# Kernel tuning notes

Measured on AMD Instinct MI355X. Metric: run time of the kernel, lower is better.

The kernel has to match this reference:

```python
import jax, jax.numpy as jnp
import numpy as np

B, N_BG, F = 512, 10000, 32
H = 128  # n_neurons


def setup_inputs() -> dict:
    key = jax.random.key(0)
    ks = jax.random.split(key, 8)
    s = lambda fan_in: 1.0 / np.sqrt(fan_in)
    return {
        "X": jax.random.normal(ks[0], (B, F), dtype=jnp.float32),
        "x_background": jax.random.normal(ks[1], (N_BG, F), dtype=jnp.float32),
        "y_background": jax.random.normal(ks[2], (N_BG, 1), dtype=jnp.float32),
        "W0": jax.random.normal(ks[3], (F, H), dtype=jnp.float32) * s(F),
        "b0": jnp.zeros((H,), dtype=jnp.float32),
        "W1": jax.random.normal(ks[4], (H, H), dtype=jnp.float32) * s(H),
        "b1": jnp.zeros((H,), dtype=jnp.float32),
        "Wout": jax.random.normal(ks[5], (H, F), dtype=jnp.float32) * s(H),
        "bout": jnp.zeros((F,), dtype=jnp.float32),
    }


def reference(X, x_background, y_background, W0, b0, W1, b1, Wout, bout):
    # MLPDistModel.get_b_vectors: 2 hidden ReLU layers + linear head, out_size = F
    h = jax.nn.relu(X @ W0 + b0)            # [B, H]
    h = jax.nn.relu(h @ W1 + b1)            # [B, H]
    b_vec = h @ Wout + bout                 # [B, F] (b_vectors squeezed from [B,1,F])
    # Nadaraya-Watson: weighted L1 distance to every background point
    diff = jnp.abs(X[:, None, :] - x_background[None, :, :])   # [B, N_bg, F]
    distances = jnp.sum(jnp.abs(b_vec)[:, None, :] * diff, axis=-1)  # [B, N_bg]
    weights = jnp.exp(-distances)
    weights_norm = weights / jnp.sum(weights, axis=1, keepdims=True)
    # y_background.swapaxes(0,1): [1, N_bg]; weighted average over background set
    out = jnp.sum(y_background.T * weights_norm, axis=1, keepdims=True)  # [B, 1]
    return out
```

## Files before the change

### kernel.cpp

```cpp
#include <hip/hip_runtime.h>

#define B      512
#define NBG    10000
#define F      32
#define H      128
#define PTS    20
#define NPG    500
#define RB     4
#define MLPBLK (B / RB)

__device__ __forceinline__ float qsum(float v) {
    int a = __builtin_amdgcn_update_dpp(0, __float_as_int(v), 0xB1, 0xF, 0xF, true);
    float v1 = v + __int_as_float(a);
    int b = __builtin_amdgcn_update_dpp(0, __float_as_int(v1), 0x4E, 0xF, 0xF, true);
    return v1 + __int_as_float(b);
}
__device__ __forceinline__ float psum1(float v) {
    int a = __builtin_amdgcn_update_dpp(0, __float_as_int(v), 0xB1, 0xF, 0xF, true);
    return v + __int_as_float(a);
}

__global__ __launch_bounds__(128) void prep_kernel(
    const float* __restrict__ X,
    const float* __restrict__ W0, const float* __restrict__ b0,
    const float* __restrict__ W1, const float* __restrict__ b1,
    const float* __restrict__ Wout, const float* __restrict__ bout,
    float* __restrict__ babsR)
{
    __shared__ __align__(16) float xr[RB * F];
    __shared__ __align__(16) float h0[RB * H];
    __shared__ __align__(16) float h1[RB * H];
    const int t  = threadIdx.x;
    const int r0 = blockIdx.x * RB;

    for (int i = t; i < RB * F; i += 128) {
        int r = i >> 5, f = i & 31;
        xr[r * F + f] = X[(r0 + r) * F + f];
    }
    __syncthreads();

    float acc[RB];
    #pragma unroll
    for (int r = 0; r < RB; ++r) acc[r] = b0[t];
    #pragma unroll
    for (int f4 = 0; f4 < F / 4; ++f4) {
        float wa = W0[(4*f4+0)*H + t];
        float wb = W0[(4*f4+1)*H + t];
        float wc = W0[(4*f4+2)*H + t];
        float wd = W0[(4*f4+3)*H + t];
        #pragma unroll
        for (int r = 0; r < RB; ++r) {
            float4 xv = *(const float4*)&xr[r * F + 4*f4];
            acc[r] += xv.x*wa + xv.y*wb + xv.z*wc + xv.w*wd;
        }
    }
    #pragma unroll
    for (int r = 0; r < RB; ++r) h0[r * H + t] = fmaxf(acc[r], 0.f);
    __syncthreads();

    #pragma unroll
    for (int r = 0; r < RB; ++r) acc[r] = b1[t];
    #pragma unroll 8
    for (int j4 = 0; j4 < H / 4; ++j4) {
        float wa = W1[(4*j4+0)*H + t];
        float wb = W1[(4*j4+1)*H + t];
        float wc = W1[(4*j4+2)*H + t];
        float wd = W1[(4*j4+3)*H + t];
        #pragma unroll
        for (int r = 0; r < RB; ++r) {
            float4 hv = *(const float4*)&h0[r * H + 4*j4];
            acc[r] += hv.x*wa + hv.y*wb + hv.z*wc + hv.w*wd;
        }
    }
    #pragma unroll
    for (int r = 0; r < RB; ++r) h1[r * H + t] = fmaxf(acc[r], 0.f);
    __syncthreads();

    for (int i = t; i < RB * F; i += 128) {
        int r = i >> 5, f = i & 31;
        float a = bout[f];
        #pragma unroll 8
        for (int j4 = 0; j4 < H / 4; ++j4) {
            float4 hv = *(const float4*)&h1[r * H + 4*j4];
            a += hv.x*Wout[(4*j4+0)*F + f] + hv.y*Wout[(4*j4+1)*F + f]
               + hv.z*Wout[(4*j4+2)*F + f] + hv.w*Wout[(4*j4+3)*F + f];
        }
        babsR[(r0 + r) * F + f] = fabsf(a);
    }
}

__global__ __launch_bounds__(256) void nw_partial(
    const float* __restrict__ X,
    const float* __restrict__ babsR,
    const float* __restrict__ xbg,
    const float* __restrict__ ybg,
    float* __restrict__ psw,
    float* __restrict__ pswy)
{
    __shared__ __align__(16) float ttp[PTS / 2 * F * 2];
    const int tid = threadIdx.x;
    const int fg  = tid & 3;
    const int bs  = tid >> 2;
    const int b0i = blockIdx.y * 128 + bs;
    const int b1i = b0i + 64;
    const int n0  = blockIdx.x * PTS;

    for (int i = tid; i < PTS * F; i += 256) {
        int nr = i >> 5, f = i & 31;
        ttp[(nr >> 1) * 64 + f * 2 + (nr & 1)] = xbg[n0 * F + i];
    }

    const float4 xqA0 = *(const float4*)&X[b0i * F + fg * 8];
    const float4 xqB0 = *(const float4*)&X[b0i * F + fg * 8 + 4];
    const float4 xqA1 = *(const float4*)&X[b1i * F + fg * 8];
    const float4 xqB1 = *(const float4*)&X[b1i * F + fg * 8 + 4];
    const float4 bvA0 = *(const float4*)&babsR[b0i * F + fg * 8];
    const float4 bvB0 = *(const float4*)&babsR[b0i * F + fg * 8 + 4];
    const float4 bvA1 = *(const float4*)&babsR[b1i * F + fg * 8];
    const float4 bvB1 = *(const float4*)&babsR[b1i * F + fg * 8 + 4];
    __syncthreads();

    const float4* t4 = (const float4*)ttp;
    float swp = 0.f, swyp = 0.f;

    #pragma unroll
    for (int jq = 0; jq < PTS / 4; ++jq) {
        const float4 yv = *(const float4*)&ybg[n0 + jq * 4];
        #pragma unroll
        for (int jj = 0; jj < 2; ++jj) {
            const int jp = jq * 2 + jj;
            const int base = jp * 16 + fg * 4;
            float d00 = 0.f, d10 = 0.f, d01 = 0.f, d11 = 0.f;
            {
                float4 v0 = t4[base + 0];
                float4 v1 = t4[base + 1];
                d00 += bvA0.x * fabsf(xqA0.x - v0.x);
                d10 += bvA0.x * fabsf(xqA0.x - v0.y);
                d01 += bvA1.x * fabsf(xqA1.x - v0.x);
                d11 += bvA1.x * fabsf(xqA1.x - v0.y);
                d00 += bvA0.y * fabsf(xqA0.y - v0.z);
                d10 += bvA0.y * fabsf(xqA0.y - v0.w);
                d01 += bvA1.y * fabsf(xqA1.y - v0.z);
                d11 += bvA1.y * fabsf(xqA1.y - v0.w);
                d00 += bvA0.z * fabsf(xqA0.z - v1.x);
                d10 += bvA0.z * fabsf(xqA0.z - v1.y);
                d01 += bvA1.z * fabsf(xqA1.z - v1.x);
                d11 += bvA1.z * fabsf(xqA1.z - v1.y);
                d00 += bvA0.w * fabsf(xqA0.w - v1.z);
                d10 += bvA0.w * fabsf(xqA0.w - v1.w);
                d01 += bvA1.w * fabsf(xqA1.w - v1.z);
                d11 += bvA1.w * fabsf(xqA1.w - v1.w);
            }
            {
                float4 v2 = t4[base + 2];
                float4 v3 = t4[base + 3];
                d00 += bvB0.x * fabsf(xqB0.x - v2.x);
                d10 += bvB0.x * fabsf(xqB0.x - v2.y);
                d01 += bvB1.x * fabsf(xqB1.x - v2.x);
                d11 += bvB1.x * fabsf(xqB1.x - v2.y);
                d00 += bvB0.y * fabsf(xqB0.y - v2.z);
                d10 += bvB0.y * fabsf(xqB0.y - v2.w);
                d01 += bvB1.y * fabsf(xqB1.y - v2.z);
                d11 += bvB1.y * fabsf(xqB1.y - v2.w);
                d00 += bvB0.z * fabsf(xqB0.z - v3.x);
                d10 += bvB0.z * fabsf(xqB0.z - v3.y);
                d01 += bvB1.z * fabsf(xqB1.z - v3.x);
                d11 += bvB1.z * fabsf(xqB1.z - v3.y);
                d00 += bvB0.w * fabsf(xqB0.w - v3.z);
                d10 += bvB0.w * fabsf(xqB0.w - v3.w);
                d01 += bvB1.w * fabsf(xqB1.w - v3.z);
                d11 += bvB1.w * fabsf(xqB1.w - v3.w);
            }
            d00 = qsum(d00); d10 = qsum(d10);
            d01 = qsum(d01); d11 = qsum(d11);

            float dA   = (fg & 1) ? d10 : d00;
            float dB   = (fg & 1) ? d11 : d01;
            float dsel = (fg & 2) ? dB : dA;
            float ysel = (fg & 1) ? (jj ? yv.w : yv.y) : (jj ? yv.z : yv.x);
            float w = __expf(-dsel);
            swp  += w;
            swyp += w * ysel;
        }
    }

    swp  = psum1(swp);
    swyp = psum1(swyp);

    if (fg == 0) {
        psw [blockIdx.x * B + b0i] = swp;
        pswy[blockIdx.x * B + b0i] = swyp;
    } else if (fg == 2) {
        psw [blockIdx.x * B + b1i] = swp;
        pswy[blockIdx.x * B + b1i] = swyp;
    }
}

__global__ __launch_bounds__(64) void nw_final(
    const float* __restrict__ psw,
    const float* __restrict__ pswy,
    float* __restrict__ out)
{
    const int b = blockIdx.x;
    const int t = threadIdx.x;

    float sw = 0.f, swy = 0.f;
    for (int c = t; c < NPG; c += 64) {
        sw  += psw [c * B + b];
        swy += pswy[c * B + b];
    }
    #pragma unroll
    for (int off = 32; off > 0; off >>= 1) {
        sw  += __shfl_down(sw,  off);
        swy += __shfl_down(swy, off);
    }
    if (t == 0) out[b] = swy / sw;
}

extern "C" void kernel_launch(void* const* d_in, const int* in_sizes, int n_in,
                              void* d_out, int out_size, void* d_ws, size_t ws_size,
                              hipStream_t stream)
{
    const float* X    = (const float*)d_in[0];
    const float* xbg  = (const float*)d_in[1];
    const float* ybg  = (const float*)d_in[2];
    const float* W0   = (const float*)d_in[3];
    const float* b0   = (const float*)d_in[4];
    const float* W1   = (const float*)d_in[5];
    const float* b1   = (const float*)d_in[6];
    const float* Wout = (const float*)d_in[7];
    const float* bout = (const float*)d_in[8];
    float* out = (float*)d_out;

    float* babsR = (float*)d_ws;
    float* psw   = babsR + B * F;
    float* pswy  = psw + NPG * B;

    prep_kernel<<<MLPBLK, 128, 0, stream>>>(X, W0, b0, W1, b1, Wout, bout, babsR);
    nw_partial<<<dim3(NPG, 4), 256, 0, stream>>>(X, babsR, xbg, ybg, psw, pswy);
    nw_final<<<B, 64, 0, stream>>>(psw, pswy, out);
}
```

Measured before the change: 30.23 us.

## Read background points directly from global memory instead of staging in LDS

Drops the shared-memory staging of the background tile and the block barrier in the NW partial kernel; each thread now loads its background feature slices straight from global memory through the cache, and the inner loop is only partially unrolled. It also halves the rows per block in the MLP prep kernel, giving more blocks. The aim is to remove LDS write/read traffic and the synchronisation stall, at the cost of redundant global/L1 loads across threads that share the same points.

```diff
diff --git a/kernel.cpp b/kernel.cpp
--- a/kernel.cpp
+++ b/kernel.cpp
@@ -6,7 +6,7 @@
 #define H      128
 #define PTS    20
 #define NPG    500
-#define RB     4
+#define RB     2
 #define MLPBLK (B / RB)
 
 __device__ __forceinline__ float qsum(float v) {
@@ -97,18 +97,12 @@
     float* __restrict__ psw,
     float* __restrict__ pswy)
 {
-    __shared__ __align__(16) float ttp[PTS / 2 * F * 2];
     const int tid = threadIdx.x;
     const int fg  = tid & 3;
     const int bs  = tid >> 2;
     const int b0i = blockIdx.y * 128 + bs;
     const int b1i = b0i + 64;
     const int n0  = blockIdx.x * PTS;
-
-    for (int i = tid; i < PTS * F; i += 256) {
-        int nr = i >> 5, f = i & 31;
-        ttp[(nr >> 1) * 64 + f * 2 + (nr & 1)] = xbg[n0 * F + i];
-    }
 
     const float4 xqA0 = *(const float4*)&X[b0i * F + fg * 8];
     const float4 xqB0 = *(const float4*)&X[b0i * F + fg * 8 + 4];
@@ -118,59 +112,59 @@
     const float4 bvB0 = *(const float4*)&babsR[b0i * F + fg * 8 + 4];
     const float4 bvA1 = *(const float4*)&babsR[b1i * F + fg * 8];
     const float4 bvB1 = *(const float4*)&babsR[b1i * F + fg * 8 + 4];
-    __syncthreads();
-
-    const float4* t4 = (const float4*)ttp;
+
+    const float4* __restrict__ xr4 = (const float4*)(xbg + n0 * F) + fg * 2;
+
     float swp = 0.f, swyp = 0.f;
 
-    #pragma unroll
+    #pragma unroll 2
     for (int jq = 0; jq < PTS / 4; ++jq) {
         const float4 yv = *(const float4*)&ybg[n0 + jq * 4];
         #pragma unroll
         for (int jj = 0; jj < 2; ++jj) {
             const int jp = jq * 2 + jj;
-            const int base = jp * 16 + fg * 4;
+            const float4 pA0 = xr4[jp * 16 + 0];
+            const float4 pA1 = xr4[jp * 16 + 1];
+            const float4 pB0 = xr4[jp * 16 + 8];
+            const float4 pB1 = xr4[jp * 16 + 9];
+
             float d00 = 0.f, d10 = 0.f, d01 = 0.f, d11 = 0.f;
-            {
-                float4 v0 = t4[base + 0];
-                float4 v1 = t4[base + 1];
-                d00 += bvA0.x * fabsf(xqA0.x - v0.x);
-                d10 += bvA0.x * fabsf(xqA0.x - v0.y);
-                d01 += bvA1.x * fabsf(xqA1.x - v0.x);
-                d11 += bvA1.x * fabsf(xqA1.x - v0.y);
-                d00 += bvA0.y * fabsf(xqA0.y - v0.z);
-                d10 += bvA0.y * fabsf(xqA0.y - v0.w);
-                d01 += bvA1.y * fabsf(xqA1.y - v0.z);
-                d11 += bvA1.y * fabsf(xqA1.y - v0.w);
-                d00 += bvA0.z * fabsf(xqA0.z - v1.x);
-                d10 += bvA0.z * fabsf(xqA0.z - v1.y);
-                d01 += bvA1.z * fabsf(xqA1.z - v1.x);
-                d11 += bvA1.z * fabsf(xqA1.z - v1.y);
-                d00 += bvA0.w * fabsf(xqA0.w - v1.z);
-                d10 += bvA0.w * fabsf(xqA0.w - v1.w);
-                d01 += bvA1.w * fabsf(xqA1.w - v1.z);
-                d11 += bvA1.w * fabsf(xqA1.w - v1.w);
-            }
-            {
-                float4 v2 = t4[base + 2];
-                float4 v3 = t4[base + 3];
-                d00 += bvB0.x * fabsf(xqB0.x - v2.x);
-                d10 += bvB0.x * fabsf(xqB0.x - v2.y);
-                d01 += bvB1.x * fabsf(xqB1.x - v2.x);
-                d11 += bvB1.x * fabsf(xqB1.x - v2.y);
-                d00 += bvB0.y * fabsf(xqB0.y - v2.z);
-                d10 += bvB0.y * fabsf(xqB0.y - v2.w);
-                d01 += bvB1.y * fabsf(xqB1.y - v2.z);
-                d11 += bvB1.y * fabsf(xqB1.y - v2.w);
-                d00 += bvB0.z * fabsf(xqB0.z - v3.x);
-                d10 += bvB0.z * fabsf(xqB0.z - v3.y);
-                d01 += bvB1.z * fabsf(xqB1.z - v3.x);
-                d11 += bvB1.z * fabsf(xqB1.z - v3.y);
-                d00 += bvB0.w * fabsf(xqB0.w - v3.z);
-                d10 += bvB0.w * fabsf(xqB0.w - v3.w);
-                d01 += bvB1.w * fabsf(xqB1.w - v3.z);
-                d11 += bvB1.w * fabsf(xqB1.w - v3.w);
-            }
+            d00 += bvA0.x * fabsf(xqA0.x - pA0.x);
+            d00 += bvA0.y * fabsf(xqA0.y - pA0.y);
+            d00 += bvA0.z * fabsf(xqA0.z - pA0.z);
+            d00 += bvA0.w * fabsf(xqA0.w - pA0.w);
+            d00 += bvB0.x * fabsf(xqB0.x - pA1.x);
+            d00 += bvB0.y * fabsf(xqB0.y - pA1.y);
+            d00 += bvB0.z * fabsf(xqB0.z - pA1.z);
+            d00 += bvB0.w * fabsf(xqB0.w - pA1.w);
+
+            d10 += bvA0.x * fabsf(xqA0.x - pB0.x);
+            d10 += bvA0.y * fabsf(xqA0.y - pB0.y);
+            d10 += bvA0.z * fabsf(xqA0.z - pB0.z);
+            d10 += bvA0.w * fabsf(xqA0.w - pB0.w);
+            d10 += bvB0.x * fabsf(xqB0.x - pB1.x);
+            d10 += bvB0.y * fabsf(xqB0.y - pB1.y);
+            d10 += bvB0.z * fabsf(xqB0.z - pB1.z);
+            d10 += bvB0.w * fabsf(xqB0.w - pB1.w);
+
+            d01 += bvA1.x * fabsf(xqA1.x - pA0.x);
+            d01 += bvA1.y * fabsf(xqA1.y - pA0.y);
+            d01 += bvA1.z * fabsf(xqA1.z - pA0.z);
+            d01 += bvA1.w * fabsf(xqA1.w - pA0.w);
+            d01 += bvB1.x * fabsf(xqB1.x - pA1.x);
+            d01 += bvB1.y * fabsf(xqB1.y - pA1.y);
+            d01 += bvB1.z * fabsf(xqB1.z - pA1.z);
+            d01 += bvB1.w * fabsf(xqB1.w - pA1.w);
+
+            d11 += bvA1.x * fabsf(xqA1.x - pB0.x);
+            d11 += bvA1.y * fabsf(xqA1.y - pB0.y);
+            d11 += bvA1.z * fabsf(xqA1.z - pB0.z);
+            d11 += bvA1.w * fabsf(xqA1.w - pB0.w);
+            d11 += bvB1.x * fabsf(xqB1.x - pB1.x);
+            d11 += bvB1.y * fabsf(xqB1.y - pB1.y);
+            d11 += bvB1.z * fabsf(xqB1.z - pB1.z);
+            d11 += bvB1.w * fabsf(xqB1.w - pB1.w);
+
             d00 = qsum(d00); d10 = qsum(d10);
             d01 = qsum(d01); d11 = qsum(d11);
 
```

Result: slower. 31.67 us (+4.8%).
